# Performance work log

Measured on AMD Instinct MI355X. Metric: run time of the kernel, lower is better.

Reference implementation:

```python
import jax, jax.numpy as jnp
import numpy as np

B, C, H, W = 4, 64, 64, 64
CQK = C // 8


def setup_inputs() -> dict:
    key = jax.random.key(0)
    ks = jax.random.split(key, 4)
    x = jax.random.normal(ks[0], (B, C, H, W), dtype=jnp.float32)
    Wq = jax.random.normal(ks[1], (CQK, C), dtype=jnp.float32) * (1.0 / np.sqrt(C))
    bq = jnp.zeros((CQK,), dtype=jnp.float32)
    Wk = jax.random.normal(ks[2], (CQK, C), dtype=jnp.float32) * (1.0 / np.sqrt(C))
    bk = jnp.zeros((CQK,), dtype=jnp.float32)
    Wv = jax.random.normal(ks[3], (C, C), dtype=jnp.float32) * (1.0 / np.sqrt(C))
    bv = jnp.zeros((C,), dtype=jnp.float32)
    gamma = jnp.ones((1,), dtype=jnp.float32)
    return {"x": x, "Wq": Wq, "bq": bq, "Wk": Wk, "bk": bk,
            "Wv": Wv, "bv": bv, "gamma": gamma}


def reference(x, Wq, bq, Wk, bk, Wv, bv, gamma):
    b, c, h, w = x.shape
    n = h * w
    xf = x.reshape(b, c, n)                      # [B, C, N]
    # 1x1 convs == per-pixel linear over channels
    q = jnp.einsum('oc,bcn->bon', Wq, xf) + bq[:, None]   # [B, C/8, N]
    k = jnp.einsum('oc,bcn->bon', Wk, xf) + bk[:, None]   # [B, C/8, N]
    v = jnp.einsum('oc,bcn->bon', Wv, xf) + bv[:, None]   # [B, C, N]
    # attention_map[b,i,j] = <q[:, i], k[:, j]>; softmax over j
    attn = jax.nn.softmax(jnp.einsum('bci,bcj->bij', q, k), axis=-1)  # [B, N, N]
    # out[b,c,i] = sum_j v[b,c,j] * attn[b,i,j]  (bmm(V, attn^T))
    out = jnp.einsum('bcj,bij->bci', v, attn).reshape(b, c, h, w)
    return gamma * out + x
```

## Files before the change

kernel.cpp:

```cpp
#include <hip/hip_runtime.h>
#include <hip/hip_bf16.h>
#include <math.h>

#define NPIX 4096

typedef __attribute__((ext_vector_type(8))) short s8;
typedef __attribute__((ext_vector_type(4))) float f4;
typedef __attribute__((ext_vector_type(16))) float f16v;

static __device__ __forceinline__ unsigned packbf2(float a, float b) {
    union { __hip_bfloat162 h; unsigned u; } x;
    x.h = __float22bfloat162_rn(make_float2(a, b));
    return x.u;
}
static __device__ __forceinline__ float2 unpackbf2(unsigned u) {
    float lo = __uint_as_float(u << 16);
    float hi = __uint_as_float(u & 0xffff0000u);
    return make_float2(lo, hi);
}

__global__ __launch_bounds__(512) void prep_kernel(
    const float* __restrict__ x,
    const float* __restrict__ Wq, const float* __restrict__ bq,
    const float* __restrict__ Wk, const float* __restrict__ bk,
    __hip_bfloat16* __restrict__ qbf, __hip_bfloat16* __restrict__ kbf,
    __hip_bfloat16* __restrict__ xbf)
{
    __shared__ float Xp[64][65];
    int t = threadIdx.x;
    int lane = t & 63;
    int grp  = t >> 6;
    int b  = blockIdx.x >> 6;
    int n0 = (blockIdx.x & 63) << 6;

    const float* xb = x + ((size_t)b << 18);
    __hip_bfloat16* xbb = xbf + ((size_t)b << 18);
#pragma unroll
    for (int u = 0; u < 8; ++u) {
        int c = grp + u * 8;
        float v = xb[((size_t)c << 12) + n0 + lane];
        Xp[c][lane] = v;
        xbb[((size_t)c << 12) + n0 + lane] = __float2bfloat16(v);
    }
    __syncthreads();

    float qa = bq[grp], ka = bk[grp];
    const float* wq = Wq + grp * 64;
    const float* wk = Wk + grp * 64;
#pragma unroll
    for (int c = 0; c < 64; ++c) {
        float xv = Xp[c][lane];
        qa = fmaf(wq[c], xv, qa);
        ka = fmaf(wk[c], xv, ka);
    }
    qa *= 1.4426950408889634f;
    int pix = b * NPIX + n0 + lane;
    qbf[(size_t)pix * 8 + grp] = __float2bfloat16(qa);
    kbf[(size_t)pix * 8 + grp] = __float2bfloat16(ka);
}

__global__ __launch_bounds__(256, 4) void flash_part_kernel(
    const __hip_bfloat16* __restrict__ qbf, const __hip_bfloat16* __restrict__ kbf,
    const __hip_bfloat16* __restrict__ xbf,
    __hip_bfloat16* __restrict__ Opart, float* __restrict__ Lp)
{
    __shared__ __align__(16) char pool[34816];
    unsigned short* Xs  = (unsigned short*)pool;
    unsigned short* PTs = (unsigned short*)(pool + 17408);

    int t = threadIdx.x;
    int w    = t >> 6;
    int lane = t & 63;
    int l32  = lane & 31;
    int lh   = lane >> 5;
    int chalf = w & 1;
    int ihalf = w >> 1;

    int blk  = blockIdx.x;
    int sId  = blk >> 8;
    int rest = blk & 255;
    int b    = rest >> 6;
    int i0   = (rest & 63) << 6;
    int jbase = sId << 10;
    int phase = (sId << 1) & 7;

    const s8 zero8 = {0, 0, 0, 0, 0, 0, 0, 0};

    s8 qf[2];
#pragma unroll
    for (int it32 = 0; it32 < 2; ++it32) {
        s8 qv = *(const s8*)(qbf + ((size_t)(b * NPIX + i0 + it32 * 32 + l32) << 3));
        qf[it32] = (lh == 0) ? qv : zero8;
    }

    f16v acc;
#pragma unroll
    for (int r = 0; r < 16; ++r) acc[r] = 0.f;
    f16v zero16;
#pragma unroll
    for (int r = 0; r < 16; ++r) zero16[r] = 0.f;
    float l[2] = {0.f, 0.f};

    const __hip_bfloat16* kb = kbf + ((size_t)(b * NPIX) << 3);
    const unsigned short* xg = (const unsigned short*)xbf + ((size_t)b << 18);

    for (int tt = 0; tt < 8; ++tt) {
        int tile = (tt + phase) & 7;
        int j0 = jbase + (tile << 7);

        __syncthreads();

        int c = t >> 2, seg = t & 3;
        const uint4* src = (const uint4*)(xg + ((size_t)c << 12) + j0 + seg * 32);
        uint4 sv0 = src[0], sv1 = src[1], sv2 = src[2], sv3 = src[3];
        s8 kf = *(const s8*)(kb + ((size_t)(j0 + w * 32 + l32) << 3));

        {
            uint4* dst = (uint4*)(Xs + c * 136 + seg * 32);
            dst[0] = sv0; dst[1] = sv1; dst[2] = sv2; dst[3] = sv3;
        }

#pragma unroll
        for (int it32 = 0; it32 < 2; ++it32) {
            f16v sv = __builtin_amdgcn_mfma_f32_32x32x16_bf16(kf, qf[it32], zero16, 0, 0, 0);
            int i = it32 * 32 + l32;
            float ls = 0.f;
#pragma unroll
            for (int g = 0; g < 4; ++g) {
                float e0 = exp2f(sv[4 * g + 0]);
                float e1 = exp2f(sv[4 * g + 1]);
                float e2 = exp2f(sv[4 * g + 2]);
                float e3 = exp2f(sv[4 * g + 3]);
                ls += (e0 + e1) + (e2 + e3);
                uint2 pk;
                pk.x = packbf2(e0, e1); pk.y = packbf2(e2, e3);
                *(uint2*)(PTs + i * 136 + w * 32 + 8 * g + 4 * lh) = pk;
            }
            l[it32] += ls;
        }
        __syncthreads();

#pragma unroll
        for (int q = 0; q < 8; ++q) {
            s8 xf = *(const s8*)(Xs  + (chalf * 32 + l32) * 136 + q * 16 + lh * 8);
            s8 pf = *(const s8*)(PTs + (ihalf * 32 + l32) * 136 + q * 16 + lh * 8);
            acc = __builtin_amdgcn_mfma_f32_32x32x16_bf16(xf, pf, acc, 0, 0, 0);
        }
    }

    float* Osh = (float*)pool;
    float* Lsh = (float*)(pool + 17408);

#pragma unroll
    for (int it32 = 0; it32 < 2; ++it32)
        l[it32] += __shfl_xor(l[it32], 32);

    __syncthreads();
    if (lh == 0) {
#pragma unroll
        for (int it32 = 0; it32 < 2; ++it32)
            Lsh[w * 64 + it32 * 32 + l32] = l[it32];
    }
    {
        int i = ihalf * 32 + l32;
#pragma unroll
        for (int r = 0; r < 16; ++r) {
            int cc = chalf * 32 + (r & 3) + 8 * (r >> 2) + 4 * lh;
            Osh[i * 68 + cc] = acc[r];
        }
    }
    __syncthreads();

    if (t < 64)
        Lp[(size_t)blk * 64 + t] = Lsh[t] + Lsh[64 + t] + Lsh[128 + t] + Lsh[192 + t];

    {
        int i = t >> 2, c0 = (t & 3) << 4;
        const float* src = Osh + i * 68 + c0;
        uint4 lo, hi;
        lo.x = packbf2(src[0], src[1]);   lo.y = packbf2(src[2], src[3]);
        lo.z = packbf2(src[4], src[5]);   lo.w = packbf2(src[6], src[7]);
        hi.x = packbf2(src[8], src[9]);   hi.y = packbf2(src[10], src[11]);
        hi.z = packbf2(src[12], src[13]); hi.w = packbf2(src[14], src[15]);
        uint4* dst = (uint4*)(Opart + (size_t)blk * 4096 + i * 64 + c0);
        dst[0] = lo; dst[1] = hi;
    }
}

__global__ __launch_bounds__(512) void merge_kernel(
    const __hip_bfloat16* __restrict__ Opart, const float* __restrict__ Lp,
    const float* __restrict__ Wv, const float* __restrict__ bv,
    const float* __restrict__ x, const float* __restrict__ gamma,
    float* __restrict__ out)
{
    __shared__ float Osh[64 * 68];
    __shared__ float Wvs[4096];
    __shared__ float LinvS[64];
    __shared__ float bvs[64];

    int t = threadIdx.x;
    int b  = blockIdx.x >> 6;
    int i0 = (blockIdx.x & 63) << 6;

    if (t < 64) {
        int i = t;
        float lt = Lp[(size_t)(0 * 256 + blockIdx.x) * 64 + i]
                 + Lp[(size_t)(1 * 256 + blockIdx.x) * 64 + i]
                 + Lp[(size_t)(2 * 256 + blockIdx.x) * 64 + i]
                 + Lp[(size_t)(3 * 256 + blockIdx.x) * 64 + i];
        LinvS[i] = 1.0f / lt;
        bvs[i] = bv[i];
    }
    {
        const float4* wsrc = (const float4*)Wv;
        float4* wdst = (float4*)Wvs;
        wdst[t] = wsrc[t];
        wdst[t + 512] = wsrc[t + 512];
    }
    __syncthreads();

    {
        int i = t >> 3, c0 = (t & 7) << 3;
        float o[8];
#pragma unroll
        for (int k = 0; k < 8; ++k) o[k] = 0.f;
#pragma unroll
        for (int sId = 0; sId < 4; ++sId) {
            size_t base = (size_t)(sId * 256 + blockIdx.x) * 4096 + i * 64 + c0;
            uint4 pk = *(const uint4*)(Opart + base);
            float2 e0 = unpackbf2(pk.x), e1 = unpackbf2(pk.y);
            float2 e2 = unpackbf2(pk.z), e3 = unpackbf2(pk.w);
            o[0] += e0.x; o[1] += e0.y; o[2] += e1.x; o[3] += e1.y;
            o[4] += e2.x; o[5] += e2.y; o[6] += e3.x; o[7] += e3.y;
        }
        float* dst = Osh + i * 68 + c0;
        *(float4*)(dst + 0) = make_float4(o[0], o[1], o[2], o[3]);
        *(float4*)(dst + 4) = make_float4(o[4], o[5], o[6], o[7]);
    }
    __syncthreads();

    {
        int i  = t & 63;
        int cg = t >> 6;
        float inv = LinvS[i];
        float res[8];
#pragma unroll
        for (int k = 0; k < 8; ++k) res[k] = 0.f;
#pragma unroll 4
        for (int cb = 0; cb < 16; ++cb) {
            float4 o = *(const float4*)(Osh + i * 68 + cb * 4);
#pragma unroll
            for (int k = 0; k < 8; ++k) {
                float4 wv4 = *(const float4*)(Wvs + (cg * 8 + k) * 64 + cb * 4);
                res[k] = fmaf(wv4.x, o.x, fmaf(wv4.y, o.y, fmaf(wv4.z, o.z, fmaf(wv4.w, o.w, res[k]))));
            }
        }
        float g = gamma[0];
        const float* xr = x + ((size_t)b << 18) + i0;
        float* outp = out + ((size_t)b << 18) + i0;
#pragma unroll
        for (int k = 0; k < 8; ++k) {
            int c = cg * 8 + k;
            float attn = fmaf(res[k], inv, bvs[c]);
            size_t off = ((size_t)c << 12) + i;
            outp[off] = fmaf(g, attn, xr[off]);
        }
    }
}

extern "C" void kernel_launch(void* const* d_in, const int* in_sizes, int n_in,
                              void* d_out, int out_size, void* d_ws, size_t ws_size,
                              hipStream_t stream) {
    const float* x     = (const float*)d_in[0];
    const float* Wq    = (const float*)d_in[1];
    const float* bq    = (const float*)d_in[2];
    const float* Wk    = (const float*)d_in[3];
    const float* bk    = (const float*)d_in[4];
    const float* Wv    = (const float*)d_in[5];
    const float* bv    = (const float*)d_in[6];
    const float* gamma = (const float*)d_in[7];
    float* out = (float*)d_out;

    __hip_bfloat16* qbf   = (__hip_bfloat16*)d_ws;
    __hip_bfloat16* kbf   = qbf + (size_t)4 * NPIX * 8;
    __hip_bfloat16* xbf   = kbf + (size_t)4 * NPIX * 8;
    __hip_bfloat16* Opart = xbf + (size_t)4 * NPIX * 64;
    float* Lp = (float*)(Opart + (size_t)1024 * 4096);

    prep_kernel<<<256, 512, 0, stream>>>(x, Wq, bq, Wk, bk, qbf, kbf, xbf);
    flash_part_kernel<<<1024, 256, 0, stream>>>(qbf, kbf, xbf, Opart, Lp);
    merge_kernel<<<256, 512, 0, stream>>>(Opart, Lp, Wv, bv, x, gamma, out);
}
```

Measured before the change: 110.7 us.

## Prefetch next tile in flash loop and rebalance prep and merge block shapes

The flash kernel now issues the global loads for the next X/K tile into registers right after the barrier, so they overlap the PV MFMA loop instead of sitting on the critical path at the top of each iteration. The per-split phase rotation is dropped. The prep kernel switches to 256 threads, each computing two Q/K outputs and writing them as packed bf16 pairs. The merge kernel uses 32-pixel tiles with 256 threads across 512 blocks for more parallelism. Prefetching adds register pressure under the 4-waves occupancy bound, and the last iteration issues a redundant load.

Result: no change. 109.9 us (-0.7%).

```diff
diff --git a/kernel.cpp b/kernel.cpp
--- a/kernel.cpp
+++ b/kernel.cpp
@@ -5,7 +5,6 @@
 #define NPIX 4096
 
 typedef __attribute__((ext_vector_type(8))) short s8;
-typedef __attribute__((ext_vector_type(4))) float f4;
 typedef __attribute__((ext_vector_type(16))) float f16v;
 
 static __device__ __forceinline__ unsigned packbf2(float a, float b) {
@@ -19,7 +18,7 @@
     return make_float2(lo, hi);
 }
 
-__global__ __launch_bounds__(512) void prep_kernel(
+__global__ __launch_bounds__(256) void prep_kernel(
     const float* __restrict__ x,
     const float* __restrict__ Wq, const float* __restrict__ bq,
     const float* __restrict__ Wk, const float* __restrict__ bk,
@@ -36,27 +35,33 @@
     const float* xb = x + ((size_t)b << 18);
     __hip_bfloat16* xbb = xbf + ((size_t)b << 18);
 #pragma unroll
-    for (int u = 0; u < 8; ++u) {
-        int c = grp + u * 8;
+    for (int u = 0; u < 16; ++u) {
+        int c = grp + u * 4;
         float v = xb[((size_t)c << 12) + n0 + lane];
         Xp[c][lane] = v;
         xbb[((size_t)c << 12) + n0 + lane] = __float2bfloat16(v);
     }
     __syncthreads();
 
-    float qa = bq[grp], ka = bk[grp];
-    const float* wq = Wq + grp * 64;
-    const float* wk = Wk + grp * 64;
+    int o0 = grp * 2, o1 = o0 + 1;
+    float qa0 = bq[o0], qa1 = bq[o1], ka0 = bk[o0], ka1 = bk[o1];
+    const float* wq0 = Wq + o0 * 64; const float* wq1 = Wq + o1 * 64;
+    const float* wk0 = Wk + o0 * 64; const float* wk1 = Wk + o1 * 64;
 #pragma unroll
     for (int c = 0; c < 64; ++c) {
         float xv = Xp[c][lane];
-        qa = fmaf(wq[c], xv, qa);
-        ka = fmaf(wk[c], xv, ka);
-    }
-    qa *= 1.4426950408889634f;
+        qa0 = fmaf(wq0[c], xv, qa0);
+        qa1 = fmaf(wq1[c], xv, qa1);
+        ka0 = fmaf(wk0[c], xv, ka0);
+        ka1 = fmaf(wk1[c], xv, ka1);
+    }
+    qa0 *= 1.4426950408889634f;
+    qa1 *= 1.4426950408889634f;
     int pix = b * NPIX + n0 + lane;
-    qbf[(size_t)pix * 8 + grp] = __float2bfloat16(qa);
-    kbf[(size_t)pix * 8 + grp] = __float2bfloat16(ka);
+    *(__hip_bfloat162*)(qbf + (size_t)pix * 8 + o0) =
+        __float22bfloat162_rn(make_float2(qa0, qa1));
+    *(__hip_bfloat162*)(kbf + (size_t)pix * 8 + o0) =
+        __float22bfloat162_rn(make_float2(ka0, ka1));
 }
 
 __global__ __launch_bounds__(256, 4) void flash_part_kernel(
@@ -82,7 +87,6 @@
     int b    = rest >> 6;
     int i0   = (rest & 63) << 6;
     int jbase = sId << 10;
-    int phase = (sId << 1) & 7;
 
     const s8 zero8 = {0, 0, 0, 0, 0, 0, 0, 0};
 
@@ -104,16 +108,18 @@
     const __hip_bfloat16* kb = kbf + ((size_t)(b * NPIX) << 3);
     const unsigned short* xg = (const unsigned short*)xbf + ((size_t)b << 18);
 
-    for (int tt = 0; tt < 8; ++tt) {
-        int tile = (tt + phase) & 7;
-        int j0 = jbase + (tile << 7);
-
+    int c = t >> 2, seg = t & 3;
+
+    uint4 sv0, sv1, sv2, sv3;
+    s8 kf;
+    {
+        const uint4* src = (const uint4*)(xg + ((size_t)c << 12) + jbase + seg * 32);
+        sv0 = src[0]; sv1 = src[1]; sv2 = src[2]; sv3 = src[3];
+        kf = *(const s8*)(kb + ((size_t)(jbase + w * 32 + l32) << 3));
+    }
+
+    for (int tile = 0; tile < 8; ++tile) {
         __syncthreads();
-
-        int c = t >> 2, seg = t & 3;
-        const uint4* src = (const uint4*)(xg + ((size_t)c << 12) + j0 + seg * 32);
-        uint4 sv0 = src[0], sv1 = src[1], sv2 = src[2], sv3 = src[3];
-        s8 kf = *(const s8*)(kb + ((size_t)(j0 + w * 32 + l32) << 3));
 
         {
             uint4* dst = (uint4*)(Xs + c * 136 + seg * 32);
@@ -140,6 +146,13 @@
         }
         __syncthreads();
 
+        {
+            int jn = jbase + (((tile + 1) & 7) << 7);
+            const uint4* src = (const uint4*)(xg + ((size_t)c << 12) + jn + seg * 32);
+            sv0 = src[0]; sv1 = src[1]; sv2 = src[2]; sv3 = src[3];
+            kf = *(const s8*)(kb + ((size_t)(jn + w * 32 + l32) << 3));
+        }
+
 #pragma unroll
         for (int q = 0; q < 8; ++q) {
             s8 xf = *(const s8*)(Xs  + (chalf * 32 + l32) * 136 + q * 16 + lh * 8);
@@ -187,46 +200,52 @@
     }
 }
 
-__global__ __launch_bounds__(512) void merge_kernel(
+__global__ __launch_bounds__(256) void merge_kernel(
     const __hip_bfloat16* __restrict__ Opart, const float* __restrict__ Lp,
     const float* __restrict__ Wv, const float* __restrict__ bv,
     const float* __restrict__ x, const float* __restrict__ gamma,
     float* __restrict__ out)
 {
-    __shared__ float Osh[64 * 68];
+    __shared__ float Osh[32 * 68];
     __shared__ float Wvs[4096];
-    __shared__ float LinvS[64];
+    __shared__ float LinvS[32];
     __shared__ float bvs[64];
 
     int t = threadIdx.x;
-    int b  = blockIdx.x >> 6;
-    int i0 = (blockIdx.x & 63) << 6;
-
-    if (t < 64) {
-        int i = t;
-        float lt = Lp[(size_t)(0 * 256 + blockIdx.x) * 64 + i]
-                 + Lp[(size_t)(1 * 256 + blockIdx.x) * 64 + i]
-                 + Lp[(size_t)(2 * 256 + blockIdx.x) * 64 + i]
-                 + Lp[(size_t)(3 * 256 + blockIdx.x) * 64 + i];
-        LinvS[i] = 1.0f / lt;
-        bvs[i] = bv[i];
-    }
+    int m  = blockIdx.x;
+    int b  = m >> 7;
+    int i0 = (m & 127) << 5;
+
+    if (t < 32) {
+        int gi = i0 + t;
+        int fb = b * 64 + (gi >> 6);
+        int r  = gi & 63;
+        float lt = Lp[(size_t)(0 * 256 + fb) * 64 + r]
+                 + Lp[(size_t)(1 * 256 + fb) * 64 + r]
+                 + Lp[(size_t)(2 * 256 + fb) * 64 + r]
+                 + Lp[(size_t)(3 * 256 + fb) * 64 + r];
+        LinvS[t] = 1.0f / lt;
+    }
+    if (t < 64) bvs[t] = bv[t];
     {
         const float4* wsrc = (const float4*)Wv;
         float4* wdst = (float4*)Wvs;
-        wdst[t] = wsrc[t];
-        wdst[t + 512] = wsrc[t + 512];
+#pragma unroll
+        for (int u = 0; u < 4; ++u) wdst[t + u * 256] = wsrc[t + u * 256];
     }
     __syncthreads();
 
     {
         int i = t >> 3, c0 = (t & 7) << 3;
+        int gi = i0 + i;
+        int fb = b * 64 + (gi >> 6);
+        int r  = gi & 63;
         float o[8];
 #pragma unroll
         for (int k = 0; k < 8; ++k) o[k] = 0.f;
 #pragma unroll
         for (int sId = 0; sId < 4; ++sId) {
-            size_t base = (size_t)(sId * 256 + blockIdx.x) * 4096 + i * 64 + c0;
+            size_t base = (size_t)(sId * 256 + fb) * 4096 + r * 64 + c0;
             uint4 pk = *(const uint4*)(Opart + base);
             float2 e0 = unpackbf2(pk.x), e1 = unpackbf2(pk.y);
             float2 e2 = unpackbf2(pk.z), e3 = unpackbf2(pk.w);
@@ -240,8 +259,8 @@
     __syncthreads();
 
     {
-        int i  = t & 63;
-        int cg = t >> 6;
+        int i  = t & 31;
+        int cg = t >> 5;
         float inv = LinvS[i];
         float res[8];
 #pragma unroll
@@ -260,9 +279,9 @@
         float* outp = out + ((size_t)b << 18) + i0;
 #pragma unroll
         for (int k = 0; k < 8; ++k) {
-            int c = cg * 8 + k;
-            float attn = fmaf(res[k], inv, bvs[c]);
-            size_t off = ((size_t)c << 12) + i;
+            int cch = cg * 8 + k;
+            float attn = fmaf(res[k], inv, bvs[cch]);
+            size_t off = ((size_t)cch << 12) + i;
             outp[off] = fmaf(g, attn, xr[off]);
         }
     }
@@ -287,7 +306,7 @@
     __hip_bfloat16* Opart = xbf + (size_t)4 * NPIX * 64;
     float* Lp = (float*)(Opart + (size_t)1024 * 4096);
 
-    prep_kernel<<<256, 512, 0, stream>>>(x, Wq, bq, Wk, bk, qbf, kbf, xbf);
+    prep_kernel<<<256, 256, 0, stream>>>(x, Wq, bq, Wk, bk, qbf, kbf, xbf);
     flash_part_kernel<<<1024, 256, 0, stream>>>(qbf, kbf, xbf, Opart, Lp);
-    merge_kernel<<<256, 512, 0, stream>>>(Opart, Lp, Wv, bv, x, gamma, out);
-}
+    merge_kernel<<<512, 256, 0, stream>>>(Opart, Lp, Wv, bv, x, gamma, out);
+}
```
